# Performance work log

Hardware: AMD Instinct MI355X
Metric: run time of the kernel (lower is better)

## Reference

```python
import jax, jax.numpy as jnp
import numpy as np

B, C, NP, DM, H, TOPK = 16, 1024, 512, 512, 8, 16
D = DM // H  # d_head = 64


def _topk_mask(scores, k):
    """Binary mask keeping top-k entries per last-dim row. scores: (..., C)."""
    shape = scores.shape
    c = shape[-1]
    k = min(k, c)
    _, idx = jax.lax.top_k(scores, k)            # (..., k)
    flat = scores.reshape(-1, c)
    idxf = idx.reshape(-1, k)
    rows = jnp.arange(flat.shape[0])[:, None]
    mask = jnp.zeros_like(flat).at[rows, idxf].set(1.0)
    return mask.reshape(shape)


def setup_inputs() -> dict:
    key = jax.random.key(0)
    ks = jax.random.split(key, 7)
    M = jax.random.normal(ks[0], (B, C, NP), dtype=jnp.float32)
    s_in = 1.0 / np.sqrt(NP)
    Wq = jax.random.uniform(ks[1], (DM, NP), jnp.float32, -s_in, s_in)
    Wk = jax.random.uniform(ks[2], (DM, NP), jnp.float32, -s_in, s_in)
    Wv = jax.random.uniform(ks[3], (DM, NP), jnp.float32, -s_in, s_in)
    s_out = 1.0 / np.sqrt(DM)
    Wo = jax.random.uniform(ks[4], (NP, DM), jnp.float32, -s_out, s_out)
    bo = jax.random.uniform(ks[5], (NP,), jnp.float32, -s_out, s_out)
    gate = jnp.asarray(1.0, dtype=jnp.float32)
    return {"M": M, "Wq": Wq, "Wk": Wk, "Wv": Wv, "Wo": Wo, "bo": bo, "gate": gate}


def reference(M, Wq, Wk, Wv, Wo, bo, gate):
    # projections: torch Linear(no bias) -> M @ W.T
    def proj(W):
        x = jnp.einsum('bcn,dn->bcd', M, W)          # (B, C, DM)
        return x.reshape(B, C, H, D).transpose(0, 2, 1, 3)  # (B, H, C, D)

    q, k, v = proj(Wq), proj(Wk), proj(Wv)
    scale = D ** -0.5
    scores = jnp.einsum('bhid,bhjd->bhij', q, k) * scale     # (B, H, C, C)

    sparse_mask = jax.lax.stop_gradient(_topk_mask(scores, TOPK))
    neg_inf = jnp.finfo(scores.dtype).min
    masked = jnp.where(sparse_mask == 0, neg_inf, scores)
    attn = jnp.nan_to_num(jax.nn.softmax(masked, axis=-1))

    out = jnp.einsum('bhij,bhjd->bhid', attn, v)             # (B, H, C, D)
    out = out.transpose(0, 2, 1, 3).reshape(B, C, DM)        # (B, C, DM)
    delta = out @ Wo.T + bo                                  # (B, C, NP); dropout is eval-mode identity
    M_tilde = M + gate * delta

    avg_scores = scores.mean(axis=1)                         # (B, C, C)
    A = _topk_mask(avg_scores, TOPK)
    return M_tilde, A
```

## Files before the change

kernel.cpp:

```cpp
#include <hip/hip_runtime.h>
#include <hip/hip_bf16.h>

#define B_  16
#define C_  1024
#define NP_ 512
#define DM_ 512
#define H_  8
#define D_  64
#define BC_ 16384

#define PAVG_STRIDE 17
#define NBMAX 4
#define FLDS 40

typedef unsigned long long ull;
typedef unsigned short u16;
using short8 = __attribute__((ext_vector_type(8))) short;
using half8  = __attribute__((ext_vector_type(8))) _Float16;
using f32x4  = __attribute__((ext_vector_type(4))) float;

__device__ __forceinline__ u16 f2bf(float x) {
    __hip_bfloat16 h = __float2bfloat16(x);
    return *reinterpret_cast<u16*>(&h);
}
__device__ __forceinline__ float bf2f(u16 v) {
    return __uint_as_float(((unsigned)v) << 16);
}
__device__ __forceinline__ u16 h_bits(_Float16 h) {
    return *reinterpret_cast<u16*>(&h);
}


__device__ __forceinline__ void hsplit_stage(const u16* __restrict__ Ah, const u16* __restrict__ Al,
    const u16* __restrict__ Bh, const u16* __restrict__ Bl,
    int lda, int ldb, int row0, int col0, int k0,
    u16* __restrict__ sAh, u16* __restrict__ sAl,
    u16* __restrict__ sBh, u16* __restrict__ sBl, int tid)
{
#pragma unroll
    for (int rep = 0; rep < 2; ++rep) {
        const int c = tid + rep * 256;
        const int row = c >> 2, kq = (c & 3) * 8;
        const size_t ga = (size_t)(row0 + row) * lda + k0 + kq;
        const size_t gb = (size_t)(col0 + row) * ldb + k0 + kq;
        *(uint4*)(&sAh[row * FLDS + kq]) = *(const uint4*)(Ah + ga);
        *(uint4*)(&sAl[row * FLDS + kq]) = *(const uint4*)(Al + ga);
        *(uint4*)(&sBh[row * FLDS + kq]) = *(const uint4*)(Bh + gb);
        *(uint4*)(&sBl[row * FLDS + kq]) = *(const uint4*)(Bl + gb);
    }
}

__device__ __forceinline__ void hsplit_compute(const u16* __restrict__ sAh, const u16* __restrict__ sAl,
    const u16* __restrict__ sBh, const u16* __restrict__ sBl,
    int lane, int wm, int wn, f32x4 (&acc)[4][4])
{
    const int q8 = (lane >> 4) * 8, l16 = lane & 15;
    half8 bh[4], bl_[4];
#pragma unroll
    for (int nt = 0; nt < 4; ++nt) {
        const int o = (wn * 64 + nt * 16 + l16) * FLDS + q8;
        bh[nt]  = *(const half8*)(&sBh[o]);
        bl_[nt] = *(const half8*)(&sBl[o]);
    }
#pragma unroll
    for (int mt = 0; mt < 4; ++mt) {
        const int o = (wm * 64 + mt * 16 + l16) * FLDS + q8;
        const half8 ah = *(const half8*)(&sAh[o]);
        const half8 al = *(const half8*)(&sAl[o]);
#pragma unroll
        for (int nt = 0; nt < 4; ++nt) {
            acc[mt][nt] = __builtin_amdgcn_mfma_f32_16x16x32_f16(ah, bh[nt],  acc[mt][nt], 0, 0, 0);
            acc[mt][nt] = __builtin_amdgcn_mfma_f32_16x16x32_f16(al, bh[nt],  acc[mt][nt], 0, 0, 0);
            acc[mt][nt] = __builtin_amdgcn_mfma_f32_16x16x32_f16(ah, bl_[nt], acc[mt][nt], 0, 0, 0);
            acc[mt][nt] = __builtin_amdgcn_mfma_f32_16x16x32_f16(al, bl_[nt], acc[mt][nt], 0, 0, 0);
        }
    }
}


__global__ __launch_bounds__(256) void f32_to_bf16(const float* __restrict__ S, u16* __restrict__ Dp)
{
    const int i = (blockIdx.x * 256 + threadIdx.x) * 4;
    const float4 v = *(const float4*)(S + i);
    ushort4 o;
    o.x = f2bf(v.x); o.y = f2bf(v.y); o.z = f2bf(v.z); o.w = f2bf(v.w);
    *(ushort4*)(Dp + i) = o;
}

__global__ __launch_bounds__(256) void f32_split_f16(const float* __restrict__ X,
    u16* __restrict__ Hh, u16* __restrict__ Hl)
{
    const int i = (blockIdx.x * 256 + threadIdx.x) * 4;
    const float4 v = *(const float4*)(X + i);
    ushort4 oh, ol;
    {
        _Float16 h = (_Float16)v.x; oh.x = h_bits(h); ol.x = h_bits((_Float16)(v.x - (float)h));
    }{
        _Float16 h = (_Float16)v.y; oh.y = h_bits(h); ol.y = h_bits((_Float16)(v.y - (float)h));
    }{
        _Float16 h = (_Float16)v.z; oh.z = h_bits(h); ol.z = h_bits((_Float16)(v.z - (float)h));
    }{
        _Float16 h = (_Float16)v.w; oh.w = h_bits(h); ol.w = h_bits((_Float16)(v.w - (float)h));
    }
    *(ushort4*)(Hh + i) = oh;
    *(ushort4*)(Hl + i) = ol;
}

__global__ __launch_bounds__(256) void mi_convert(const float* __restrict__ X,
    u16* __restrict__ Bb, u16* __restrict__ Hh, u16* __restrict__ Hl)
{
    const int i = (blockIdx.x * 256 + threadIdx.x) * 4;
    const float4 v = *(const float4*)(X + i);
    ushort4 ob, oh, ol;
    {
        _Float16 h = (_Float16)v.x; ob.x = f2bf(v.x); oh.x = h_bits(h); ol.x = h_bits((_Float16)(v.x - (float)h));
    }{
        _Float16 h = (_Float16)v.y; ob.y = f2bf(v.y); oh.y = h_bits(h); ol.y = h_bits((_Float16)(v.y - (float)h));
    }{
        _Float16 h = (_Float16)v.z; ob.z = f2bf(v.z); oh.z = h_bits(h); ol.z = h_bits((_Float16)(v.z - (float)h));
    }{
        _Float16 h = (_Float16)v.w; ob.w = f2bf(v.w); oh.w = h_bits(h); ol.w = h_bits((_Float16)(v.w - (float)h));
    }
    *(ushort4*)(Bb + i) = ob;
    *(ushort4*)(Hh + i) = oh;
    *(ushort4*)(Hl + i) = ol;
}

__global__ __launch_bounds__(256) void qk_gemm_mfma(
    const u16* __restrict__ Mih, const u16* __restrict__ Mil,
    const u16* __restrict__ Wqh, const u16* __restrict__ Wql,
    const u16* __restrict__ Wkh, const u16* __restrict__ Wkl,
    u16* __restrict__ Qh, u16* __restrict__ Ql,
    u16* __restrict__ Kh, u16* __restrict__ Kl)
{
    __shared__ u16 sAh[128 * FLDS];
    __shared__ u16 sAl[128 * FLDS];
    __shared__ u16 sBh[128 * FLDS];
    __shared__ u16 sBl[128 * FLDS];

    const int tid = threadIdx.x, lane = tid & 63, w = tid >> 6;
    const int wm = w >> 1, wn = w & 1;
    const int z = blockIdx.z;
    const u16* Bh = z ? Wkh : Wqh;
    const u16* Bl = z ? Wkl : Wql;
    u16* outH = z ? Kh : Qh;
    u16* outL = z ? Kl : Ql;
    const int row0 = blockIdx.x * 128, col0 = blockIdx.y * 128;

    f32x4 acc[4][4];
#pragma unroll
    for (int mt = 0; mt < 4; ++mt)
#pragma unroll
        for (int nt = 0; nt < 4; ++nt)
            acc[mt][nt] = (f32x4){0.f, 0.f, 0.f, 0.f};

    for (int k0 = 0; k0 < NP_; k0 += 32) {
        hsplit_stage(Mih, Mil, Bh, Bl, NP_, NP_, row0, col0, k0, sAh, sAl, sBh, sBl, tid);
        __syncthreads();
        hsplit_compute(sAh, sAl, sBh, sBl, lane, wm, wn, acc);
        __syncthreads();
    }

    const int quad = lane >> 4, l16 = lane & 15;
#pragma unroll
    for (int mt = 0; mt < 4; ++mt)
#pragma unroll
        for (int nt = 0; nt < 4; ++nt) {
            const int n = col0 + wn * 64 + nt * 16 + l16;
            const int hh = n >> 6, dd = n & 63;
#pragma unroll
            for (int reg = 0; reg < 4; ++reg) {
                const int m = row0 + wm * 64 + mt * 16 + quad * 4 + reg;
                const int bl = m >> 10, c = m & 1023;
                const size_t idx = ((size_t)(bl * 8 + hh) * C_ + c) * D_ + dd;
                const float v = acc[mt][nt][reg];
                const _Float16 vh = (_Float16)v;
                outH[idx] = h_bits(vh);
                outL[idx] = h_bits((_Float16)(v - (float)vh));
            }
        }
}

__global__ __launch_bounds__(256) void score_gemm_mfma(
    const u16* __restrict__ Qh, const u16* __restrict__ Ql,
    const u16* __restrict__ Kh, const u16* __restrict__ Kl,
    float* __restrict__ S)
{
    __shared__ u16 sAh[128 * FLDS];
    __shared__ u16 sAl[128 * FLDS];
    __shared__ u16 sBh[128 * FLDS];
    __shared__ u16 sBl[128 * FLDS];

    const int tid = threadIdx.x, lane = tid & 63, w = tid >> 6;
    const int wm = w >> 1, wn = w & 1;
    const int z = blockIdx.z;
    const size_t off = (size_t)z * C_ * D_;
    const u16* Ah = Qh + off;  const u16* Al = Ql + off;
    const u16* Bh = Kh + off;  const u16* Bl = Kl + off;
    float* Cp = S + (size_t)z * C_ * C_;
    const int row0 = blockIdx.x * 128, col0 = blockIdx.y * 128;

    f32x4 acc[4][4];
#pragma unroll
    for (int mt = 0; mt < 4; ++mt)
#pragma unroll
        for (int nt = 0; nt < 4; ++nt)
            acc[mt][nt] = (f32x4){0.f, 0.f, 0.f, 0.f};

    for (int k0 = 0; k0 < D_; k0 += 32) {
        hsplit_stage(Ah, Al, Bh, Bl, D_, D_, row0, col0, k0, sAh, sAl, sBh, sBl, tid);
        __syncthreads();
        hsplit_compute(sAh, sAl, sBh, sBl, lane, wm, wn, acc);
        __syncthreads();
    }

    const int quad = lane >> 4, l16 = lane & 15;
#pragma unroll
    for (int mt = 0; mt < 4; ++mt)
#pragma unroll
        for (int nt = 0; nt < 4; ++nt) {
            const int n = col0 + wn * 64 + nt * 16 + l16;
#pragma unroll
            for (int reg = 0; reg < 4; ++reg) {
                const int m = row0 + wm * 64 + mt * 16 + quad * 4 + reg;
                Cp[(size_t)m * C_ + n] = acc[mt][nt][reg] * 0.125f;
            }
        }
}

__global__ __launch_bounds__(256) void v_gemm_mfma(const u16* __restrict__ Mib,
    const u16* __restrict__ Wvb, u16* __restrict__ Vb)
{
    __shared__ u16 As[128 * FLDS];
    __shared__ u16 Bs[128 * FLDS];
    const int tid = threadIdx.x, lane = tid & 63, w = tid >> 6;
    const int wm = w >> 1, wn = w & 1;
    const int row0 = blockIdx.x * 128, col0 = blockIdx.y * 128;

    f32x4 acc[4][4];
#pragma unroll
    for (int mt = 0; mt < 4; ++mt)
#pragma unroll
        for (int nt = 0; nt < 4; ++nt)
            acc[mt][nt] = (f32x4){0.f, 0.f, 0.f, 0.f};

    const int q8 = (lane >> 4) * 8, l16 = lane & 15;
    for (int k0 = 0; k0 < NP_; k0 += 32) {
#pragma unroll
        for (int rep = 0; rep < 2; ++rep) {
            const int c = tid + rep * 256;
            const int row = c >> 2, kq = (c & 3) * 8;
            *(uint4*)(&As[row * FLDS + kq]) = *(const uint4*)(Mib + (size_t)(row0 + row) * NP_ + k0 + kq);
            *(uint4*)(&Bs[row * FLDS + kq]) = *(const uint4*)(Wvb + (size_t)(col0 + row) * NP_ + k0 + kq);
        }
        __syncthreads();
        short8 a[4], bfr[4];
#pragma unroll
        for (int mt = 0; mt < 4; ++mt)
            a[mt] = *(const short8*)(&As[(wm * 64 + mt * 16 + l16) * FLDS + q8]);
#pragma unroll
        for (int nt = 0; nt < 4; ++nt)
            bfr[nt] = *(const short8*)(&Bs[(wn * 64 + nt * 16 + l16) * FLDS + q8]);
#pragma unroll
        for (int mt = 0; mt < 4; ++mt)
#pragma unroll
            for (int nt = 0; nt < 4; ++nt)
                acc[mt][nt] = __builtin_amdgcn_mfma_f32_16x16x32_bf16(a[mt], bfr[nt], acc[mt][nt], 0, 0, 0);
        __syncthreads();
    }
    const int quad = lane >> 4;
#pragma unroll
    for (int mt = 0; mt < 4; ++mt)
#pragma unroll
        for (int nt = 0; nt < 4; ++nt) {
            const int n = col0 + wn * 64 + nt * 16 + l16;
#pragma unroll
            for (int reg = 0; reg < 4; ++reg) {
                const int m = row0 + wm * 64 + mt * 16 + quad * 4 + reg;
                Vb[(size_t)m * DM_ + n] = f2bf(acc[mt][nt][reg]);
            }
        }
}


__device__ __forceinline__ ull pack1(float f, int j) {
    unsigned b = __float_as_uint(f);
    unsigned u = b ^ ((unsigned)((int)b >> 31) | 0x80000000u);
    return ((ull)u << 32) | (unsigned)(1023 - j);
}
__device__ __forceinline__ float unpack_val(ull e) {
    unsigned u = (unsigned)(e >> 32);
    unsigned b = u ^ ((u & 0x80000000u) ? 0x80000000u : 0xFFFFFFFFu);
    return __uint_as_float(b);
}
__device__ __forceinline__ int unpack_j(ull e) {
    return 1023 - (int)(e & 0xFFFFFFFFu);
}

__device__ __forceinline__ void topk16_fast(float (&f)[16], const int lane,
                                            ull* candw, ull (&out)[16])
{
    float mv = f[0];
#pragma unroll
    for (int r = 1; r < 16; ++r) mv = fmaxf(mv, f[r]);
#pragma unroll
    for (int k = 2; k <= 64; k <<= 1) {
#pragma unroll
        for (int j = k >> 1; j > 0; j >>= 1) {
            const float t = __shfl_xor(mv, j);
            const bool kmax = ((lane & k) == 0) == ((lane & j) == 0);
            mv = kmax ? fmaxf(mv, t) : fminf(mv, t);
        }
    }
    const float tau = __shfl(mv, 15);
    unsigned msk = 0u;
#pragma unroll
    for (int r = 0; r < 16; ++r) msk |= (f[r] >= tau) ? (1u << r) : 0u;
    const int cnt = __popc(msk);
    int incl = cnt;
#pragma unroll
    for (int off = 1; off < 64; off <<= 1) {
        const int t = __shfl_up(incl, off);
        incl += (lane >= off) ? t : 0;
    }
    const int total = __shfl(incl, 63);

    if (total <= 64) {
        int ofs = incl - cnt;
        unsigned m = msk;
        while (m) {
            const int r = __ffs(m) - 1;
            m &= m - 1;
            candw[ofs++] = pack1(f[r], (lane << 4) + r);
        }
        ull e = candw[lane];
        if (lane >= total) e = 0ull;
#pragma unroll
        for (int k = 2; k <= 64; k <<= 1) {
#pragma unroll
            for (int j = k >> 1; j > 0; j >>= 1) {
                const ull p = __shfl_xor(e, j);
                const bool kmax = ((lane & k) == 0) == ((lane & j) == 0);
                if ((p > e) == kmax) e = p;
            }
        }
#pragma unroll
        for (int t = 0; t < 16; ++t) out[t] = __shfl(e, t);
    } else {
        for (int it = 0; it < 16; ++it) {
            float bv = f[0]; int bj = lane << 4;
#pragma unroll
            for (int r = 1; r < 16; ++r)
                if (f[r] > bv) { bv = f[r]; bj = (lane << 4) + r; }
#pragma unroll
            for (int off = 32; off >= 1; off >>= 1) {
                const float ov = __shfl_xor(bv, off);
                const int   oj = __shfl_xor(bj, off);
                if (ov > bv || (ov == bv && oj < bj)) { bv = ov; bj = oj; }
            }
            out[it] = pack1(bv, bj);
            if ((bj >> 4) == lane) f[bj & 15] = -3.402823466e38f;
        }
    }
}

__device__ __forceinline__ ull topk16_serial(float (&f)[16], const int lane)
{
    ull e = 0ull;
    for (int it = 0; it < 16; ++it) {
        float bv = f[0]; int bj = lane << 4;
#pragma unroll
        for (int r = 1; r < 16; ++r)
            if (f[r] > bv) { bv = f[r]; bj = (lane << 4) + r; }
#pragma unroll
        for (int off = 32; off >= 1; off >>= 1) {
            const float ov = __shfl_xor(bv, off);
            const int   oj = __shfl_xor(bj, off);
            if (ov > bv || (ov == bv && oj < bj)) { bv = ov; bj = oj; }
        }
        if (lane == it) e = pack1(bv, bj);
        if ((bj >> 4) == lane) f[bj & 15] = -3.402823466e38f;
    }
    return e;
}

__device__ __forceinline__ void topk16_dual(float (&fA)[16], float (&fB)[16],
                                            const int lane, ull* cwA, ull* cwB,
                                            ull &eA, ull &eB)
{
    float mA = fA[0], mB = fB[0];
#pragma unroll
    for (int r = 1; r < 16; ++r) { mA = fmaxf(mA, fA[r]); mB = fmaxf(mB, fB[r]); }
#pragma unroll
    for (int k = 2; k <= 64; k <<= 1) {
#pragma unroll
        for (int j = k >> 1; j > 0; j >>= 1) {
            const float tA = __shfl_xor(mA, j);
            const float tB = __shfl_xor(mB, j);
            const bool kmax = ((lane & k) == 0) == ((lane & j) == 0);
            mA = kmax ? fmaxf(mA, tA) : fminf(mA, tA);
            mB = kmax ? fmaxf(mB, tB) : fminf(mB, tB);
        }
    }
    const float tauA = __shfl(mA, 15);
    const float tauB = __shfl(mB, 15);
    unsigned mskA = 0u, mskB = 0u;
#pragma unroll
    for (int r = 0; r < 16; ++r) {
        mskA |= (fA[r] >= tauA) ? (1u << r) : 0u;
        mskB |= (fB[r] >= tauB) ? (1u << r) : 0u;
    }
    const int cntA = __popc(mskA), cntB = __popc(mskB);
    int inclA = cntA, inclB = cntB;
#pragma unroll
    for (int off = 1; off < 64; off <<= 1) {
        const int tA = __shfl_up(inclA, off);
        const int tB = __shfl_up(inclB, off);
        inclA += (lane >= off) ? tA : 0;
        inclB += (lane >= off) ? tB : 0;
    }
    const int totalA = __shfl(inclA, 63);
    const int totalB = __shfl(inclB, 63);

    if (totalA <= 64) {
        int ofs = inclA - cntA;
        unsigned m = mskA;
        while (m) {
            const int r = __ffs(m) - 1;
            m &= m - 1;
            cwA[ofs++] = pack1(fA[r], (lane << 4) + r);
        }
    }
    if (totalB <= 64) {
        int ofs = inclB - cntB;
        unsigned m = mskB;
        while (m) {
            const int r = __ffs(m) - 1;
            m &= m - 1;
            cwB[ofs++] = pack1(fB[r], (lane << 4) + r);
        }
    }
    eA = (totalA <= 64 && lane < totalA) ? cwA[lane] : 0ull;
    eB = (totalB <= 64 && lane < totalB) ? cwB[lane] : 0ull;
#pragma unroll
    for (int k = 2; k <= 64; k <<= 1) {
#pragma unroll
        for (int j = k >> 1; j > 0; j >>= 1) {
            const ull pA = __shfl_xor(eA, j);
            const ull pB = __shfl_xor(eB, j);
            const bool kmax = ((lane & k) == 0) == ((lane & j) == 0);
            if ((pA > eA) == kmax) eA = pA;
            if ((pB > eB) == kmax) eB = pB;
        }
    }
    if (totalA > 64) eA = topk16_serial(fA, lane);
    if (totalB > 64) eB = topk16_serial(fB, lane);
}

__device__ __forceinline__ void attn_out(const ull e, const u16* __restrict__ V,
                                         int bl, int i, int h, int lane,
                                         u16* __restrict__ O)
{
    float vals[16]; int jl[16];
#pragma unroll
    for (int t = 0; t < 16; ++t) {
        const ull et = __shfl(e, t);
        vals[t] = unpack_val(et);
        jl[t]   = unpack_j(et);
    }
    const float mx = vals[0];
    float wv[16];
    float Z = 0.0f;
#pragma unroll
    for (int t = 0; t < 16; ++t) { wv[t] = __expf(vals[t] - mx); Z += wv[t]; }
    const float inv = 1.0f / Z;
#pragma unroll
    for (int t = 0; t < 16; ++t) wv[t] *= inv;
    float o = 0.0f;
#pragma unroll
    for (int t = 0; t < 16; ++t)
        o = fmaf(wv[t], bf2f(V[((size_t)(bl * C_ + jl[t])) * DM_ + h * D_ + lane]), o);
    O[((size_t)(bl * C_ + i)) * DM_ + h * D_ + lane] = f2bf(o);
}

__global__ __launch_bounds__(320) void topk_attn(const float* __restrict__ S,
    const u16* __restrict__ V, u16* __restrict__ O,
    float* __restrict__ Aout, int b0)
{
    __shared__ float pavg[4 * 64 * PAVG_STRIDE];
    __shared__ ull   cand[4][2][64];
    __shared__ ull   candA[64];

    const int tid = threadIdx.x, lane = tid & 63, w = tid >> 6;
    const int rb = blockIdx.x, bl = rb >> 10, i = rb & 1023;
    const int b = b0 + bl;

    float f1[16], f2[16];
    if (w < 4) {
        const float* r1 = S + ((size_t)(bl * 8 + w) * C_ + i) * C_ + lane * 16;
        const float* r2 = S + ((size_t)(bl * 8 + w + 4) * C_ + i) * C_ + lane * 16;
#pragma unroll
        for (int q = 0; q < 4; ++q) {
            const float4 x = *(const float4*)(r1 + q * 4);
            f1[q * 4 + 0] = x.x; f1[q * 4 + 1] = x.y; f1[q * 4 + 2] = x.z; f1[q * 4 + 3] = x.w;
            const float4 y = *(const float4*)(r2 + q * 4);
            f2[q * 4 + 0] = y.x; f2[q * 4 + 1] = y.y; f2[q * 4 + 2] = y.z; f2[q * 4 + 3] = y.w;
        }
        float* pw = pavg + w * 64 * PAVG_STRIDE + lane * PAVG_STRIDE;
#pragma unroll
        for (int r = 0; r < 16; ++r) pw[r] = f1[r] + f2[r];
    }
    __syncthreads();

    if (w < 4) {
        ull eA, eB;
        topk16_dual(f1, f2, lane, cand[w][0], cand[w][1], eA, eB);
        attn_out(eA, V, bl, i, w,     lane, O);
        attn_out(eB, V, bl, i, w + 4, lane, O);
    } else {
        float fa[16];
#pragma unroll
        for (int r = 0; r < 16; ++r) {
            fa[r] = pavg[0 * 64 * PAVG_STRIDE + lane * PAVG_STRIDE + r]
                  + pavg[1 * 64 * PAVG_STRIDE + lane * PAVG_STRIDE + r]
                  + pavg[2 * 64 * PAVG_STRIDE + lane * PAVG_STRIDE + r]
                  + pavg[3 * 64 * PAVG_STRIDE + lane * PAVG_STRIDE + r];
        }
        ull top[16];
        topk16_fast(fa, lane, candA, top);
        unsigned mybits = 0u;
#pragma unroll
        for (int t = 0; t < 16; ++t) {
            const int j = unpack_j(top[t]);
            if ((j >> 4) == lane) mybits |= 1u << (j & 15);
        }
        float* arow = Aout + ((size_t)(b * C_ + i)) * C_ + lane * 16;
#pragma unroll
        for (int q = 0; q < 4; ++q) {
            float4 o4;
            o4.x = ((mybits >> (q * 4 + 0)) & 1u) ? 1.0f : 0.0f;
            o4.y = ((mybits >> (q * 4 + 1)) & 1u) ? 1.0f : 0.0f;
            o4.z = ((mybits >> (q * 4 + 2)) & 1u) ? 1.0f : 0.0f;
            o4.w = ((mybits >> (q * 4 + 3)) & 1u) ? 1.0f : 0.0f;
            *(float4*)(arow + q * 4) = o4;
        }
    }
}

__global__ __launch_bounds__(256) void final_gemm_mfma(const u16* __restrict__ O,
    const u16* __restrict__ Wob, const float* __restrict__ Mi,
    const float* __restrict__ bo, const float* __restrict__ gatep,
    float* __restrict__ out)
{
    __shared__ u16 As[128 * FLDS];
    __shared__ u16 Bs[128 * FLDS];
    const int tid = threadIdx.x, lane = tid & 63, w = tid >> 6;
    const int wm = w >> 1, wn = w & 1;
    const int row0 = blockIdx.x * 128, col0 = blockIdx.y * 128;

    f32x4 acc[4][4];
#pragma unroll
    for (int mt = 0; mt < 4; ++mt)
#pragma unroll
        for (int nt = 0; nt < 4; ++nt)
            acc[mt][nt] = (f32x4){0.f, 0.f, 0.f, 0.f};

    const int q8 = (lane >> 4) * 8, l16 = lane & 15;
    for (int k0 = 0; k0 < DM_; k0 += 32) {
#pragma unroll
        for (int rep = 0; rep < 2; ++rep) {
            const int c = tid + rep * 256;
            const int row = c >> 2, kq = (c & 3) * 8;
            *(uint4*)(&As[row * FLDS + kq]) = *(const uint4*)(O   + (size_t)(row0 + row) * DM_ + k0 + kq);
            *(uint4*)(&Bs[row * FLDS + kq]) = *(const uint4*)(Wob + (size_t)(col0 + row) * DM_ + k0 + kq);
        }
        __syncthreads();
        short8 a[4], bfr[4];
#pragma unroll
        for (int mt = 0; mt < 4; ++mt)
            a[mt] = *(const short8*)(&As[(wm * 64 + mt * 16 + l16) * FLDS + q8]);
#pragma unroll
        for (int nt = 0; nt < 4; ++nt)
            bfr[nt] = *(const short8*)(&Bs[(wn * 64 + nt * 16 + l16) * FLDS + q8]);
#pragma unroll
        for (int mt = 0; mt < 4; ++mt)
#pragma unroll
            for (int nt = 0; nt < 4; ++nt)
                acc[mt][nt] = __builtin_amdgcn_mfma_f32_16x16x32_bf16(a[mt], bfr[nt], acc[mt][nt], 0, 0, 0);
        __syncthreads();
    }

    const float g = gatep[0];
    const int quad = lane >> 4;
#pragma unroll
    for (int mt = 0; mt < 4; ++mt) {
#pragma unroll
        for (int nt = 0; nt < 4; ++nt) {
            const int n = col0 + wn * 64 + nt * 16 + l16;
            const float bon = bo[n];
#pragma unroll
            for (int reg = 0; reg < 4; ++reg) {
                const int m = row0 + wm * 64 + mt * 16 + quad * 4 + reg;
                out[(size_t)m * NP_ + n] = Mi[(size_t)m * NP_ + n] + g * (acc[mt][nt][reg] + bon);
            }
        }
    }
}

extern "C" void kernel_launch(void* const* d_in, const int* in_sizes, int n_in,
                              void* d_out, int out_size, void* d_ws, size_t ws_size,
                              hipStream_t stream)
{
    (void)in_sizes; (void)n_in; (void)out_size;
    const float* Mi   = (const float*)d_in[0];
    const float* Wq   = (const float*)d_in[1];
    const float* Wk   = (const float*)d_in[2];
    const float* Wv   = (const float*)d_in[3];
    const float* Wo   = (const float*)d_in[4];
    const float* bo   = (const float*)d_in[5];
    const float* gate = (const float*)d_in[6];
    float* out  = (float*)d_out;
    float* Aout = out + (size_t)BC_ * NP_;

    char* p = (char*)d_ws;
    const size_t SZ_W   = (size_t)NP_ * DM_ * 2;
    const size_t SZ_BIG = (size_t)BC_ * DM_ * 2;
    u16* Wob = (u16*)p; p += SZ_W;
    u16* Wvb = (u16*)p; p += SZ_W;
    u16* Wqh = (u16*)p; p += SZ_W;
    u16* Wql = (u16*)p; p += SZ_W;
    u16* Wkh = (u16*)p; p += SZ_W;
    u16* Wkl = (u16*)p; p += SZ_W;
    u16* Mib = (u16*)p; p += SZ_BIG;
    u16* Mih = (u16*)p; p += SZ_BIG;
    u16* Mil = (u16*)p; p += SZ_BIG;
    u16* Qh  = (u16*)p; p += SZ_BIG;
    u16* Ql  = (u16*)p; p += SZ_BIG;
    u16* Kh  = (u16*)p; p += SZ_BIG;
    u16* Kl  = (u16*)p; p += SZ_BIG;
    u16* Vb  = (u16*)p; p += SZ_BIG;
    u16* Of  = (u16*)p; p += SZ_BIG;
    float* Sc = (float*)p;

    const size_t fixed = 6 * SZ_W + 9 * SZ_BIG;
    const size_t chunk_bytes = (size_t)H_ * C_ * C_ * 4;
    size_t availB = (ws_size > fixed) ? (ws_size - fixed) : 0;
    int NB = (int)(availB / chunk_bytes);
    if (NB < 1) NB = 1;
    if (NB > NBMAX) NB = NBMAX;

    f32_to_bf16<<<dim3(NP_ * DM_ / 1024), 256, 0, stream>>>(Wo, Wob);
    f32_to_bf16<<<dim3(NP_ * DM_ / 1024), 256, 0, stream>>>(Wv, Wvb);
    f32_split_f16<<<dim3(NP_ * DM_ / 1024), 256, 0, stream>>>(Wq, Wqh, Wql);
    f32_split_f16<<<dim3(NP_ * DM_ / 1024), 256, 0, stream>>>(Wk, Wkh, Wkl);
    mi_convert<<<dim3((int)((size_t)BC_ * NP_ / 1024)), 256, 0, stream>>>(Mi, Mib, Mih, Mil);

    qk_gemm_mfma<<<dim3(BC_ / 128, DM_ / 128, 2), 256, 0, stream>>>(
        Mih, Mil, Wqh, Wql, Wkh, Wkl, Qh, Ql, Kh, Kl);
    v_gemm_mfma<<<dim3(BC_ / 128, DM_ / 128), 256, 0, stream>>>(Mib, Wvb, Vb);

    for (int b0 = 0; b0 < B_; b0 += NB) {
        const int nb = (B_ - b0 < NB) ? (B_ - b0) : NB;
        const size_t hoff = (size_t)b0 * H_ * C_ * D_;
        score_gemm_mfma<<<dim3(C_ / 128, C_ / 128, nb * 8), 256, 0, stream>>>(
            Qh + hoff, Ql + hoff, Kh + hoff, Kl + hoff, Sc);
        topk_attn<<<dim3(nb * C_), 320, 0, stream>>>(
            Sc, Vb + (size_t)b0 * C_ * DM_, Of + (size_t)b0 * C_ * DM_, Aout, b0);
    }

    final_gemm_mfma<<<dim3(BC_ / 128, NP_ / 128), 256, 0, stream>>>(
        Of, Wob, Mi, bo, gate, out);
}
```

Before: 644.8 us.

## Replace bitonic sort top-k with ballot-based radix select

Replaces the per-wave bitonic sorts, used both to find the 16th-largest lane max and to sort the candidates, with a bitwise radix select built on ballot and popcount. Selected entries are compacted into shared memory for the attention-output step, and the paired dual-row top-k is replaced by two sequential single-row selections. The goal is to drop the long chains of cross-lane shuffles. In exchange it runs up to 42 serial ballot steps per selection and loses the interleaving of the two rows.

```diff
diff --git a/kernel.cpp b/kernel.cpp
--- a/kernel.cpp
+++ b/kernel.cpp
@@ -296,23 +296,51 @@
 __device__ __forceinline__ int unpack_j(ull e) {
     return 1023 - (int)(e & 0xFFFFFFFFu);
 }
-
-__device__ __forceinline__ void topk16_fast(float (&f)[16], const int lane,
-                                            ull* candw, ull (&out)[16])
+__device__ __forceinline__ unsigned mono32(float f) {
+    unsigned b = __float_as_uint(f);
+    return b ^ ((unsigned)((int)b >> 31) | 0x80000000u);
+}
+__device__ __forceinline__ float mono32_inv(unsigned u) {
+    unsigned b = u ^ ((u & 0x80000000u) ? 0x80000000u : 0xFFFFFFFFu);
+    return __uint_as_float(b);
+}
+
+__device__ __forceinline__ unsigned radix16_u32(unsigned k)
+{
+    unsigned p = 0u;
+#pragma unroll
+    for (int b = 31; b >= 0; --b) {
+        const unsigned t = p | (1u << b);
+        if (__popcll(__ballot(k >= t)) >= 16) p = t;
+    }
+    return p;
+}
+
+__device__ __forceinline__ ull radix16_u64(ull e)
+{
+    ull p = 0ull;
+#pragma unroll
+    for (int b = 63; b >= 32; --b) {
+        const ull t = p | (1ull << b);
+        if (__popcll(__ballot(e >= t)) >= 16) p = t;
+    }
+#pragma unroll
+    for (int b = 9; b >= 0; --b) {
+        const ull t = p | (1ull << b);
+        if (__popcll(__ballot(e >= t)) >= 16) p = t;
+    }
+    return p;
+}
+
+template<bool FILLW>
+__device__ __forceinline__ unsigned select16(float (&f)[16], const int lane,
+                                             ull* candw, ull* wsl)
 {
     float mv = f[0];
 #pragma unroll
     for (int r = 1; r < 16; ++r) mv = fmaxf(mv, f[r]);
-#pragma unroll
-    for (int k = 2; k <= 64; k <<= 1) {
-#pragma unroll
-        for (int j = k >> 1; j > 0; j >>= 1) {
-            const float t = __shfl_xor(mv, j);
-            const bool kmax = ((lane & k) == 0) == ((lane & j) == 0);
-            mv = kmax ? fmaxf(mv, t) : fminf(mv, t);
-        }
-    }
-    const float tau = __shfl(mv, 15);
+    const float tau = mono32_inv(radix16_u32(mono32(mv)));
+
     unsigned msk = 0u;
 #pragma unroll
     for (int r = 0; r < 16; ++r) msk |= (f[r] >= tau) ? (1u << r) : 0u;
@@ -333,20 +361,33 @@
             m &= m - 1;
             candw[ofs++] = pack1(f[r], (lane << 4) + r);
         }
-        ull e = candw[lane];
-        if (lane >= total) e = 0ull;
-#pragma unroll
-        for (int k = 2; k <= 64; k <<= 1) {
-#pragma unroll
-            for (int j = k >> 1; j > 0; j >>= 1) {
-                const ull p = __shfl_xor(e, j);
-                const bool kmax = ((lane & k) == 0) == ((lane & j) == 0);
-                if ((p > e) == kmax) e = p;
+        const ull e = (lane < total) ? candw[lane] : 0ull;
+        const ull kmin = radix16_u64(e);
+
+        unsigned wbits = 0u;
+#pragma unroll
+        for (int r = 0; r < 16; ++r)
+            wbits |= (pack1(f[r], (lane << 4) + r) >= kmin) ? (1u << r) : 0u;
+
+        if (FILLW) {
+            const int wcnt = __popc(wbits);
+            int winc = wcnt;
+#pragma unroll
+            for (int off = 1; off < 64; off <<= 1) {
+                const int t = __shfl_up(winc, off);
+                winc += (lane >= off) ? t : 0;
             }
-        }
-#pragma unroll
-        for (int t = 0; t < 16; ++t) out[t] = __shfl(e, t);
+            int wofs = winc - wcnt;
+            unsigned wm = wbits;
+            while (wm) {
+                const int r = __ffs(wm) - 1;
+                wm &= wm - 1;
+                wsl[wofs++] = pack1(f[r], (lane << 4) + r);
+            }
+        }
+        return wbits;
     } else {
+        unsigned wbits = 0u;
         for (int it = 0; it < 16; ++it) {
             float bv = f[0]; int bj = lane << 4;
 #pragma unroll
@@ -358,128 +399,36 @@
                 const int   oj = __shfl_xor(bj, off);
                 if (ov > bv || (ov == bv && oj < bj)) { bv = ov; bj = oj; }
             }
-            out[it] = pack1(bv, bj);
-            if ((bj >> 4) == lane) f[bj & 15] = -3.402823466e38f;
-        }
-    }
-}
-
-__device__ __forceinline__ ull topk16_serial(float (&f)[16], const int lane)
-{
-    ull e = 0ull;
-    for (int it = 0; it < 16; ++it) {
-        float bv = f[0]; int bj = lane << 4;
-#pragma unroll
-        for (int r = 1; r < 16; ++r)
-            if (f[r] > bv) { bv = f[r]; bj = (lane << 4) + r; }
-#pragma unroll
-        for (int off = 32; off >= 1; off >>= 1) {
-            const float ov = __shfl_xor(bv, off);
-            const int   oj = __shfl_xor(bj, off);
-            if (ov > bv || (ov == bv && oj < bj)) { bv = ov; bj = oj; }
-        }
-        if (lane == it) e = pack1(bv, bj);
-        if ((bj >> 4) == lane) f[bj & 15] = -3.402823466e38f;
-    }
-    return e;
-}
-
-__device__ __forceinline__ void topk16_dual(float (&fA)[16], float (&fB)[16],
-                                            const int lane, ull* cwA, ull* cwB,
-                                            ull &eA, ull &eB)
-{
-    float mA = fA[0], mB = fB[0];
-#pragma unroll
-    for (int r = 1; r < 16; ++r) { mA = fmaxf(mA, fA[r]); mB = fmaxf(mB, fB[r]); }
-#pragma unroll
-    for (int k = 2; k <= 64; k <<= 1) {
-#pragma unroll
-        for (int j = k >> 1; j > 0; j >>= 1) {
-            const float tA = __shfl_xor(mA, j);
-            const float tB = __shfl_xor(mB, j);
-            const bool kmax = ((lane & k) == 0) == ((lane & j) == 0);
-            mA = kmax ? fmaxf(mA, tA) : fminf(mA, tA);
-            mB = kmax ? fmaxf(mB, tB) : fminf(mB, tB);
-        }
-    }
-    const float tauA = __shfl(mA, 15);
-    const float tauB = __shfl(mB, 15);
-    unsigned mskA = 0u, mskB = 0u;
-#pragma unroll
-    for (int r = 0; r < 16; ++r) {
-        mskA |= (fA[r] >= tauA) ? (1u << r) : 0u;
-        mskB |= (fB[r] >= tauB) ? (1u << r) : 0u;
-    }
-    const int cntA = __popc(mskA), cntB = __popc(mskB);
-    int inclA = cntA, inclB = cntB;
-#pragma unroll
-    for (int off = 1; off < 64; off <<= 1) {
-        const int tA = __shfl_up(inclA, off);
-        const int tB = __shfl_up(inclB, off);
-        inclA += (lane >= off) ? tA : 0;
-        inclB += (lane >= off) ? tB : 0;
-    }
-    const int totalA = __shfl(inclA, 63);
-    const int totalB = __shfl(inclB, 63);
-
-    if (totalA <= 64) {
-        int ofs = inclA - cntA;
-        unsigned m = mskA;
-        while (m) {
-            const int r = __ffs(m) - 1;
-            m &= m - 1;
-            cwA[ofs++] = pack1(fA[r], (lane << 4) + r);
-        }
-    }
-    if (totalB <= 64) {
-        int ofs = inclB - cntB;
-        unsigned m = mskB;
-        while (m) {
-            const int r = __ffs(m) - 1;
-            m &= m - 1;
-            cwB[ofs++] = pack1(fB[r], (lane << 4) + r);
-        }
-    }
-    eA = (totalA <= 64 && lane < totalA) ? cwA[lane] : 0ull;
-    eB = (totalB <= 64 && lane < totalB) ? cwB[lane] : 0ull;
-#pragma unroll
-    for (int k = 2; k <= 64; k <<= 1) {
-#pragma unroll
-        for (int j = k >> 1; j > 0; j >>= 1) {
-            const ull pA = __shfl_xor(eA, j);
-            const ull pB = __shfl_xor(eB, j);
-            const bool kmax = ((lane & k) == 0) == ((lane & j) == 0);
-            if ((pA > eA) == kmax) eA = pA;
-            if ((pB > eB) == kmax) eB = pB;
-        }
-    }
-    if (totalA > 64) eA = topk16_serial(fA, lane);
-    if (totalB > 64) eB = topk16_serial(fB, lane);
-}
-
-__device__ __forceinline__ void attn_out(const ull e, const u16* __restrict__ V,
+            if (FILLW && lane == 0) wsl[it] = pack1(bv, bj);
+            if ((bj >> 4) == lane) { wbits |= 1u << (bj & 15); f[bj & 15] = -3.402823466e38f; }
+        }
+        return wbits;
+    }
+}
+
+__device__ __forceinline__ void attn_out(const ull* __restrict__ wsl, const u16* __restrict__ V,
                                          int bl, int i, int h, int lane,
                                          u16* __restrict__ O)
 {
     float vals[16]; int jl[16];
 #pragma unroll
     for (int t = 0; t < 16; ++t) {
-        const ull et = __shfl(e, t);
-        vals[t] = unpack_val(et);
-        jl[t]   = unpack_j(et);
-    }
-    const float mx = vals[0];
+        const ull e = wsl[t];
+        vals[t] = unpack_val(e);
+        jl[t]   = unpack_j(e);
+    }
+    float mx = vals[0];
+#pragma unroll
+    for (int t = 1; t < 16; ++t) mx = fmaxf(mx, vals[t]);
     float wv[16];
     float Z = 0.0f;
 #pragma unroll
     for (int t = 0; t < 16; ++t) { wv[t] = __expf(vals[t] - mx); Z += wv[t]; }
     const float inv = 1.0f / Z;
-#pragma unroll
-    for (int t = 0; t < 16; ++t) wv[t] *= inv;
     float o = 0.0f;
 #pragma unroll
     for (int t = 0; t < 16; ++t)
-        o = fmaf(wv[t], bf2f(V[((size_t)(bl * C_ + jl[t])) * DM_ + h * D_ + lane]), o);
+        o = fmaf(wv[t] * inv, bf2f(V[((size_t)(bl * C_ + jl[t])) * DM_ + h * D_ + lane]), o);
     O[((size_t)(bl * C_ + i)) * DM_ + h * D_ + lane] = f2bf(o);
 }
 
@@ -488,8 +437,8 @@
     float* __restrict__ Aout, int b0)
 {
     __shared__ float pavg[4 * 64 * PAVG_STRIDE];
-    __shared__ ull   cand[4][2][64];
-    __shared__ ull   candA[64];
+    __shared__ ull   cand[5][64];
+    __shared__ ull   wsl[4][2][16];
 
     const int tid = threadIdx.x, lane = tid & 63, w = tid >> 6;
     const int rb = blockIdx.x, bl = rb >> 10, i = rb & 1023;
@@ -513,10 +462,10 @@
     __syncthreads();
 
     if (w < 4) {
-        ull eA, eB;
-        topk16_dual(f1, f2, lane, cand[w][0], cand[w][1], eA, eB);
-        attn_out(eA, V, bl, i, w,     lane, O);
-        attn_out(eB, V, bl, i, w + 4, lane, O);
+        select16<true>(f1, lane, cand[w], wsl[w][0]);
+        select16<true>(f2, lane, cand[w], wsl[w][1]);
+        attn_out(wsl[w][0], V, bl, i, w,     lane, O);
+        attn_out(wsl[w][1], V, bl, i, w + 4, lane, O);
     } else {
         float fa[16];
 #pragma unroll
@@ -526,14 +475,7 @@
                   + pavg[2 * 64 * PAVG_STRIDE + lane * PAVG_STRIDE + r]
                   + pavg[3 * 64 * PAVG_STRIDE + lane * PAVG_STRIDE + r];
         }
-        ull top[16];
-        topk16_fast(fa, lane, candA, top);
-        unsigned mybits = 0u;
-#pragma unroll
-        for (int t = 0; t < 16; ++t) {
-            const int j = unpack_j(top[t]);
-            if ((j >> 4) == lane) mybits |= 1u << (j & 15);
-        }
+        const unsigned mybits = select16<false>(fa, lane, cand[4], cand[4]);
         float* arow = Aout + ((size_t)(b * C_ + i)) * C_ + lane * 16;
 #pragma unroll
         for (int q = 0; q < 4; ++q) {
```

Measured after the change: 695.3 us. +7.8%, slower.
